# Kernel optimization log

Hardware: AMD Instinct MI355X
Metric: run time of the kernel (lower is better)

The kernel has to match this reference:

```python
import math
import jax, jax.numpy as jnp
import numpy as np

N, E = 100000, 1600000
F_IN, HID, CLS, H = 128, 64, 40, 2  # per-head channels C = HID = 64, concat width = H*HID = 128


def _lin_params(key, fan_in, fan_out):
    kw, kb = jax.random.split(key)
    s = 1.0 / math.sqrt(fan_in)
    W = jax.random.uniform(kw, (fan_in, fan_out), minval=-s, maxval=s, dtype=jnp.float32)
    b = jax.random.uniform(kb, (fan_out,), minval=-s, maxval=s, dtype=jnp.float32)
    return W, b


def setup_inputs() -> dict:
    key = jax.random.key(0)
    ks = jax.random.split(key, 12)
    x = jax.random.normal(ks[0], (N, F_IN), dtype=jnp.float32)
    edge_index = jax.random.randint(ks[1], (2, E), 0, N, dtype=jnp.int64)
    inp = {"x": x, "edge_index": edge_index}
    # layer 1: in=F_IN(128) -> H*HID(128); layer 2: in=H*HID(128) -> H*HID(128)
    names = ["q1", "k1", "v1", "s1", "q2", "k2", "v2", "s2"]
    fans = [(F_IN, H * HID)] * 4 + [(H * HID, H * HID)] * 4
    for i, (nm, (fi, fo)) in enumerate(zip(names, fans)):
        W, b = _lin_params(ks[2 + i], fi, fo)
        inp["W" + nm] = W
        inp["b" + nm] = b
    Wlin, blin = _lin_params(ks[10], H * HID, CLS)
    inp["Wlin"], inp["blin"] = Wlin, blin
    return inp


def _tconv(x, src, dst, Wq, bq, Wk, bk, Wv, bv, Ws, bs):
    # PyG TransformerConv (concat=True, beta=False, edge_dim=None, root_weight=True)
    n = x.shape[0]
    q = (x @ Wq + bq).reshape(n, H, HID)
    k = (x @ Wk + bk).reshape(n, H, HID)
    v = (x @ Wv + bv).reshape(n, H, HID)
    # per-edge attention score: q_i (dst) dot k_j (src), per head
    alpha = jnp.einsum("ehc,ehc->eh", q[dst], k[src]) / math.sqrt(HID)  # [E, H]
    # segment softmax over incoming edges of each dst node
    m = jax.ops.segment_max(alpha, dst, num_segments=n)
    a = jnp.exp(alpha - m[dst])
    denom = jax.ops.segment_sum(a, dst, num_segments=n)
    a = a / (denom[dst] + 1e-16)
    # weighted scatter-aggregate of values
    msg = v[src] * a[:, :, None]  # [E, H, HID]
    out = jax.ops.segment_sum(msg, dst, num_segments=n).reshape(n, H * HID)
    return out + x @ Ws + bs  # root/skip connection


def reference(x, edge_index, Wq1, bq1, Wk1, bk1, Wv1, bv1, Ws1, bs1,
              Wq2, bq2, Wk2, bk2, Wv2, bv2, Ws2, bs2, Wlin, blin):
    src, dst = edge_index[0], edge_index[1]
    h = _tconv(x, src, dst, Wq1, bq1, Wk1, bk1, Wv1, bv1, Ws1, bs1)
    h = jax.nn.elu(h)  # dropout is identity in eval mode
    h = _tconv(h, src, dst, Wq2, bq2, Wk2, bk2, Wv2, bv2, Ws2, bs2)
    return h @ Wlin + blin  # [N, CLS]
```

## Files before the change

### kernel.cpp

```cpp
#include <hip/hip_runtime.h>
#include <math.h>

#define NNODES 100000
#define NEDGES 1600000
#define FD 128
#define NCLS 40
#define NB_SCAN ((NNODES + 1023) / 1024)

typedef __attribute__((ext_vector_type(8))) short short8v;
typedef __attribute__((ext_vector_type(4))) float f32x4;

__device__ __forceinline__ unsigned short f32_to_bf16_rne(float f) {
    unsigned int u = __float_as_uint(f);
    unsigned int r = u + 0x7fff + ((u >> 16) & 1);
    return (unsigned short)(r >> 16);
}
__device__ __forceinline__ float bf16_to_f32(unsigned short h) {
    return __uint_as_float(((unsigned int)h) << 16);
}


__global__ void detect_kernel(const long long* __restrict__ ei, int* __restrict__ flag_is32) {
    int t = blockIdx.x * blockDim.x + threadIdx.x;
    size_t idx = (size_t)t * (NEDGES / 4096);
    long long v = ei[idx];
    if (v < 0 || v >= NNODES) atomicOr(flag_is32, 1);
}

__device__ __forceinline__ void load_edge(const void* eiv, int is32, int e, int& s, int& d) {
    if (is32) {
        const int* p = (const int*)eiv;
        s = p[e]; d = p[NEDGES + e];
    } else {
        const long long* p = (const long long*)eiv;
        s = (int)p[e]; d = (int)p[NEDGES + e];
    }
}


__global__ void hist_kernel(const void* __restrict__ eiv, const int* __restrict__ flag_is32,
                            int* __restrict__ row_ptr) {
    int is32 = *flag_is32;
    int e = blockIdx.x * blockDim.x + threadIdx.x;
    if (e < NEDGES) {
        int s, d;
        load_edge(eiv, is32, e, s, d);
        atomicAdd(&row_ptr[d + 1], 1);
    }
}

__global__ __launch_bounds__(1024) void scan_blk(int* __restrict__ row_ptr,
                                                 int* __restrict__ cursor,
                                                 int* __restrict__ blk_tot) {
    __shared__ int wtot[16];
    __shared__ int woff[16];
    int t = threadIdx.x, lane = t & 63, wid = t >> 6;
    int i = blockIdx.x * 1024 + t;
    int c = (i < NNODES) ? row_ptr[1 + i] : 0;
    int x = c;
    #pragma unroll
    for (int off = 1; off < 64; off <<= 1) {
        int y = __shfl_up(x, off, 64);
        if (lane >= off) x += y;
    }
    if (lane == 63) wtot[wid] = x;
    __syncthreads();
    if (t < 16) {
        int v = wtot[t];
        #pragma unroll
        for (int off = 1; off < 16; off <<= 1) {
            int y = __shfl_up(v, off, 64);
            if (t >= off) v += y;
        }
        woff[t] = v;
    }
    __syncthreads();
    int excl = (wid == 0) ? 0 : woff[wid - 1];
    int incl = x + excl;
    if (i < NNODES) {
        row_ptr[1 + i] = incl;
        cursor[i]      = incl - c;
    }
    if (t == 0) blk_tot[blockIdx.x] = woff[15];
}

__global__ void scan_tops(const int* __restrict__ blk_tot, int* __restrict__ blk_off) {
    __shared__ int s[128];
    int t = threadIdx.x;
    int c0 = (t < NB_SCAN) ? blk_tot[t] : 0;
    s[t] = c0;
    __syncthreads();
    for (int d = 1; d < 128; d <<= 1) {
        int v = (t >= d) ? s[t - d] : 0;
        __syncthreads();
        s[t] += v;
        __syncthreads();
    }
    if (t < NB_SCAN) blk_off[t] = s[t] - c0;
}

__global__ __launch_bounds__(1024) void scan_add(int* __restrict__ row_ptr,
                                                 int* __restrict__ cursor,
                                                 const int* __restrict__ blk_off) {
    int i = blockIdx.x * 1024 + threadIdx.x;
    if (i < NNODES) {
        int o = blk_off[blockIdx.x];
        row_ptr[1 + i] += o;
        cursor[i]      += o;
    }
}

__global__ void fill_kernel(const void* __restrict__ eiv, const int* __restrict__ flag_is32,
                            int* __restrict__ cursor, int* __restrict__ src_sorted) {
    int is32 = *flag_is32;
    int e = blockIdx.x * blockDim.x + threadIdx.x;
    if (e < NEDGES) {
        int s, d;
        load_edge(eiv, is32, e, s, d);
        int pos = atomicAdd(&cursor[d], 1);
        src_sorted[pos] = s;
    }
}


__global__ void pack_w(const float* __restrict__ W, short* __restrict__ Whi,
                       short* __restrict__ Wlo, int slot) {
    int lane = threadIdx.x;
    int ctkk = blockIdx.x;
    int ct = ctkk >> 2, kk = ctkk & 3;
    int col = ct * 16 + (lane & 15);
    int k0 = kk * 32 + (lane >> 4) * 8;
    short8v h, l;
    #pragma unroll
    for (int j = 0; j < 8; j++) {
        float v = W[(size_t)(k0 + j) * FD + col];
        unsigned short hh = f32_to_bf16_rne(v);
        float rem = v - bf16_to_f32(hh);
        h[j] = (short)hh;
        l[j] = (short)f32_to_bf16_rne(rem);
    }
    size_t o = ((size_t)slot * 32 + ctkk) * 512 + (size_t)lane * 8;
    *(short8v*)(Whi + o) = h;
    *(short8v*)(Wlo + o) = l;
}


__global__ __launch_bounds__(256) void proj_gemm_mfma(
    const float* __restrict__ X,
    const short* __restrict__ Whi, const short* __restrict__ Wlo,
    const float* __restrict__ b0, const float* __restrict__ b1,
    const float* __restrict__ b2, const float* __restrict__ b3,
    float* __restrict__ Q, unsigned short* __restrict__ KV, float* __restrict__ SKIP)
{
    int wid = threadIdx.x >> 6, lane = threadIdx.x & 63;
    int rowbase = blockIdx.x * 64 + wid * 16;
    int r = lane & 15, q = lane >> 4;
    int row = rowbase + r;

    short8v xh[4], xl[4];
    if (row < NNODES) {
        const float* xp = X + (size_t)row * FD + q * 8;
        #pragma unroll
        for (int kk = 0; kk < 4; kk++) {
            float4 v0 = *(const float4*)(xp + kk * 32);
            float4 v1 = *(const float4*)(xp + kk * 32 + 4);
            float vv[8] = {v0.x, v0.y, v0.z, v0.w, v1.x, v1.y, v1.z, v1.w};
            #pragma unroll
            for (int j = 0; j < 8; j++) {
                unsigned short h = f32_to_bf16_rne(vv[j]);
                float rem = vv[j] - bf16_to_f32(h);
                xh[kk][j] = (short)h;
                xl[kk][j] = (short)f32_to_bf16_rne(rem);
            }
        }
    } else {
        short8v z = {0, 0, 0, 0, 0, 0, 0, 0};
        #pragma unroll
        for (int kk = 0; kk < 4; kk++) { xh[kk] = z; xl[kk] = z; }
    }

    #pragma unroll
    for (int pt = 0; pt < 4; pt++) {
        const float* bias = (pt == 0) ? b0 : (pt == 1) ? b1 : (pt == 2) ? b2 : b3;
        #pragma unroll
        for (int ct = 0; ct < 8; ct++) {
            const short* wp = Whi + ((size_t)(pt * 8 + ct) * 4) * 512 + (size_t)lane * 8;
            const short* lp = Wlo + ((size_t)(pt * 8 + ct) * 4) * 512 + (size_t)lane * 8;
            f32x4 acc = {0.f, 0.f, 0.f, 0.f};
            #pragma unroll
            for (int kk = 0; kk < 4; kk++) {
                short8v bh = *(const short8v*)(wp + kk * 512);
                short8v bl = *(const short8v*)(lp + kk * 512);
                acc = __builtin_amdgcn_mfma_f32_16x16x32_bf16(xh[kk], bh, acc, 0, 0, 0);
                acc = __builtin_amdgcn_mfma_f32_16x16x32_bf16(xl[kk], bh, acc, 0, 0, 0);
                acc = __builtin_amdgcn_mfma_f32_16x16x32_bf16(xh[kk], bl, acc, 0, 0, 0);
            }
            float bb = bias[ct * 16 + r];
            int e = ct * 16 + r;
            #pragma unroll
            for (int j = 0; j < 4; j++) {
                int ro = rowbase + q * 4 + j;
                if (ro < NNODES) {
                    float val = acc[j] + bb;
                    if (pt == 0)      Q[(size_t)ro * FD + e] = val;
                    else if (pt == 1) KV[(size_t)ro * 256 + 2 * e]     = f32_to_bf16_rne(val);
                    else if (pt == 2) KV[(size_t)ro * 256 + 2 * e + 1] = f32_to_bf16_rne(val);
                    else              SKIP[(size_t)ro * FD + e] = val;
                }
            }
        }
    }
}


__global__ __launch_bounds__(256) void agg_kernel(
    const float* __restrict__ Q, const unsigned short* __restrict__ KV,
    const float* __restrict__ SKIP, float* __restrict__ OUT,
    const int* __restrict__ row_ptr, const int* __restrict__ src_sorted, int apply_elu)
{
    int wid  = threadIdx.x >> 6;
    int lane = threadIdx.x & 63;
    int node = blockIdx.x * 4 + wid;
    if (node >= NNODES) return;
    size_t rb = (size_t)node * FD;
    float2 q = *(const float2*)(Q + rb + 2 * lane);
    q.x *= 0.125f; q.y *= 0.125f;
    float m = -INFINITY, s = 0.f;
    float accx = 0.f, accy = 0.f;
    int e0 = row_ptr[node], e1 = row_ptr[node + 1];

#define EDGE_UPD(W)                                          \
    {                                                        \
        float kx = bf16_to_f32((W).x & 0xffffu);             \
        float vx = bf16_to_f32((W).x >> 16);                 \
        float ky = bf16_to_f32((W).y & 0xffffu);             \
        float vy = bf16_to_f32((W).y >> 16);                 \
        float p = q.x * kx + q.y * ky;                       \
        p += __shfl_xor(p, 1, 64);                           \
        p += __shfl_xor(p, 2, 64);                           \
        p += __shfl_xor(p, 4, 64);                           \
        p += __shfl_xor(p, 8, 64);                           \
        p += __shfl_xor(p, 16, 64);                          \
        float mn   = fmaxf(m, p);                            \
        float corr = __expf(m - mn);                         \
        float w    = __expf(p - mn);                         \
        s    = s * corr + w;                                 \
        accx = accx * corr + w * vx;                         \
        accy = accy * corr + w * vy;                         \
        m = mn;                                              \
    }

    for (int base = e0; base < e1; base += 4) {
        int nrem = e1 - base;
        int j0 = src_sorted[base];
        int j1 = src_sorted[nrem > 1 ? base + 1 : base];
        int j2 = src_sorted[nrem > 2 ? base + 2 : base];
        int j3 = src_sorted[nrem > 3 ? base + 3 : base];
        uint2 w0 = *(const uint2*)((const unsigned int*)(KV + (size_t)j0 * 256) + 2 * lane);
        uint2 w1 = *(const uint2*)((const unsigned int*)(KV + (size_t)j1 * 256) + 2 * lane);
        uint2 w2 = *(const uint2*)((const unsigned int*)(KV + (size_t)j2 * 256) + 2 * lane);
        uint2 w3 = *(const uint2*)((const unsigned int*)(KV + (size_t)j3 * 256) + 2 * lane);
        EDGE_UPD(w0)
        if (nrem > 1) EDGE_UPD(w1)
        if (nrem > 2) EDGE_UPD(w2)
        if (nrem > 3) EDGE_UPD(w3)
    }
#undef EDGE_UPD

    float r = 1.f / (s + 1e-16f);
    float2 sk = *(const float2*)(SKIP + rb + 2 * lane);
    float ox = accx * r + sk.x;
    float oy = accy * r + sk.y;
    if (apply_elu) {
        ox = (ox > 0.f) ? ox : (__expf(ox) - 1.f);
        oy = (oy > 0.f) ? oy : (__expf(oy) - 1.f);
    }
    *(float2*)(OUT + rb + 2 * lane) = make_float2(ox, oy);
}


__global__ void final_lin(const float* __restrict__ H, const float* __restrict__ Wl,
                          const float* __restrict__ bl, float* __restrict__ out)
{
    __shared__ float ws[FD * NCLS];
    __shared__ float xs[8][FD + 1];
    int tx = threadIdx.x;
    int ty = threadIdx.y;
    int t = ty * NCLS + tx;
    for (int i = t; i < FD * NCLS; i += 320) ws[i] = Wl[i];
    int row = blockIdx.x * 8;
    for (int i = t; i < 8 * FD; i += 320) {
        int r = i >> 7, c = i & 127;
        xs[r][c] = (row + r < NNODES) ? H[(size_t)(row + r) * FD + c] : 0.f;
    }
    __syncthreads();
    float acc = bl[tx];
    #pragma unroll
    for (int k = 0; k < FD; k++) acc += xs[ty][k] * ws[k * NCLS + tx];
    if (row + ty < NNODES) out[(size_t)(row + ty) * NCLS + tx] = acc;
}


extern "C" void kernel_launch(void* const* d_in, const int* in_sizes, int n_in,
                              void* d_out, int out_size, void* d_ws, size_t ws_size,
                              hipStream_t stream) {
    const float* x  = (const float*)d_in[0];
    const void*  ei = d_in[1];
    const float* Wq1 = (const float*)d_in[2],  *bq1 = (const float*)d_in[3];
    const float* Wk1 = (const float*)d_in[4],  *bk1 = (const float*)d_in[5];
    const float* Wv1 = (const float*)d_in[6],  *bv1 = (const float*)d_in[7];
    const float* Ws1 = (const float*)d_in[8],  *bs1 = (const float*)d_in[9];
    const float* Wq2 = (const float*)d_in[10], *bq2 = (const float*)d_in[11];
    const float* Wk2 = (const float*)d_in[12], *bk2 = (const float*)d_in[13];
    const float* Wv2 = (const float*)d_in[14], *bv2 = (const float*)d_in[15];
    const float* Ws2 = (const float*)d_in[16], *bs2 = (const float*)d_in[17];
    const float* Wlin = (const float*)d_in[18], *blin = (const float*)d_in[19];
    float* out = (float*)d_out;

    const size_t BUFE = (size_t)NNODES * FD;
    float* Qb = (float*)d_ws;
    float* Cb = Qb + BUFE;
    float* Sb = Cb + BUFE;
    unsigned short* KVb = (unsigned short*)(Sb + BUFE);
    int* row_ptr    = (int*)(KVb + (size_t)NNODES * 256);
    int* cursor     = row_ptr + (NNODES + 1);
    int* src_sorted = cursor + NNODES;
    int* flag_is32  = src_sorted + NEDGES;
    int* blk_tot    = flag_is32 + 1;
    int* blk_off    = blk_tot + NB_SCAN;
    uintptr_t pal = ((uintptr_t)(blk_off + NB_SCAN) + 15) & ~(uintptr_t)15;
    short* Whi = (short*)pal;
    short* Wlo = Whi + 8 * 16384;

    const float* Ws[8] = {Wq1, Wk1, Wv1, Ws1, Wq2, Wk2, Wv2, Ws2};
    for (int s = 0; s < 8; s++)
        pack_w<<<32, 64, 0, stream>>>(Ws[s], Whi, Wlo, s);

    hipMemsetAsync(row_ptr, 0, (NNODES + 1) * sizeof(int), stream);
    hipMemsetAsync(flag_is32, 0, sizeof(int), stream);
    detect_kernel<<<16, 256, 0, stream>>>((const long long*)ei, flag_is32);
    hist_kernel<<<(NEDGES + 255) / 256, 256, 0, stream>>>(ei, flag_is32, row_ptr);
    scan_blk<<<NB_SCAN, 1024, 0, stream>>>(row_ptr, cursor, blk_tot);
    scan_tops<<<1, 128, 0, stream>>>(blk_tot, blk_off);
    scan_add<<<NB_SCAN, 1024, 0, stream>>>(row_ptr, cursor, blk_off);
    fill_kernel<<<(NEDGES + 255) / 256, 256, 0, stream>>>(ei, flag_is32, cursor, src_sorted);

    int pgrid = (NNODES + 63) / 64;

    proj_gemm_mfma<<<pgrid, 256, 0, stream>>>(x, Whi, Wlo,
        bq1, bk1, bv1, bs1, Qb, KVb, Sb);
    agg_kernel<<<(NNODES + 3) / 4, 256, 0, stream>>>(Qb, KVb, Sb, Qb,
        row_ptr, src_sorted, 1);

    proj_gemm_mfma<<<pgrid, 256, 0, stream>>>(Qb, Whi + 4 * 16384, Wlo + 4 * 16384,
        bq2, bk2, bv2, bs2, Cb, KVb, Sb);
    agg_kernel<<<(NNODES + 3) / 4, 256, 0, stream>>>(Cb, KVb, Sb, Cb,
        row_ptr, src_sorted, 0);

    final_lin<<<(NNODES + 7) / 8, dim3(NCLS, 8), 0, stream>>>(Cb, Wlin, blin, out);
}
```

Measured before the change: 947.0 us.

## Process two edges per wavefront in agg kernel and drop online softmax max

The aggregation kernel splits each 64-lane wavefront into two 32-lane halves. Each half handles a different edge and loads 16-byte uint4 K/V chunks, where each lane previously loaded 8 bytes. The online-softmax running max and its rescaling are removed, so each edge needs one exp and four shuffles instead of two exps and five. A final cross-half shuffle combines the partial sums. This removes the serial max dependency and halves the shuffle reductions per edge, but without max subtraction exp can overflow when attention scores are large.

Result: faster. 906.7 us (-4.2%).

```diff
diff --git a/kernel.cpp b/kernel.cpp
--- a/kernel.cpp
+++ b/kernel.cpp
@@ -220,62 +220,72 @@
 {
     int wid  = threadIdx.x >> 6;
     int lane = threadIdx.x & 63;
+    int half = lane >> 5;
+    int sub  = lane & 31;
     int node = blockIdx.x * 4 + wid;
     if (node >= NNODES) return;
     size_t rb = (size_t)node * FD;
-    float2 q = *(const float2*)(Q + rb + 2 * lane);
-    q.x *= 0.125f; q.y *= 0.125f;
-    float m = -INFINITY, s = 0.f;
-    float accx = 0.f, accy = 0.f;
+
+    float4 q4 = *(const float4*)(Q + rb + sub * 4);
+    q4.x *= 0.125f; q4.y *= 0.125f; q4.z *= 0.125f; q4.w *= 0.125f;
+
+    float s = 0.f;
+    float4 acc = make_float4(0.f, 0.f, 0.f, 0.f);
     int e0 = row_ptr[node], e1 = row_ptr[node + 1];
-
-#define EDGE_UPD(W)                                          \
-    {                                                        \
-        float kx = bf16_to_f32((W).x & 0xffffu);             \
-        float vx = bf16_to_f32((W).x >> 16);                 \
-        float ky = bf16_to_f32((W).y & 0xffffu);             \
-        float vy = bf16_to_f32((W).y >> 16);                 \
-        float p = q.x * kx + q.y * ky;                       \
-        p += __shfl_xor(p, 1, 64);                           \
-        p += __shfl_xor(p, 2, 64);                           \
-        p += __shfl_xor(p, 4, 64);                           \
-        p += __shfl_xor(p, 8, 64);                           \
-        p += __shfl_xor(p, 16, 64);                          \
-        float mn   = fmaxf(m, p);                            \
-        float corr = __expf(m - mn);                         \
-        float w    = __expf(p - mn);                         \
-        s    = s * corr + w;                                 \
-        accx = accx * corr + w * vx;                         \
-        accy = accy * corr + w * vy;                         \
-        m = mn;                                              \
+    const uint4* KV4 = (const uint4*)KV;
+
+#define PAIR_UPD(EID)                                                          \
+    {                                                                          \
+        int eid = (EID);                                                       \
+        int valid = eid < e1;                                                  \
+        int j = src_sorted[valid ? eid : e1 - 1];                              \
+        uint4 wv = KV4[(size_t)j * 32 + sub];                                  \
+        float kx = __uint_as_float(wv.x << 16);                                \
+        float vx = __uint_as_float(wv.x & 0xffff0000u);                        \
+        float ky = __uint_as_float(wv.y << 16);                                \
+        float vy = __uint_as_float(wv.y & 0xffff0000u);                        \
+        float kz = __uint_as_float(wv.z << 16);                                \
+        float vz = __uint_as_float(wv.z & 0xffff0000u);                        \
+        float kw = __uint_as_float(wv.w << 16);                                \
+        float vw = __uint_as_float(wv.w & 0xffff0000u);                        \
+        float p = q4.x * kx + q4.y * ky + q4.z * kz + q4.w * kw;               \
+        p += __shfl_xor(p, 1, 64);                                             \
+        p += __shfl_xor(p, 2, 64);                                             \
+        p += __shfl_xor(p, 4, 64);                                             \
+        p += __shfl_xor(p, 8, 64);           \
+        float w = valid ? __expf(p) : 0.f;                                     \
+        s += w;                                                                \
+        acc.x += w * vx; acc.y += w * vy;                                      \
+        acc.z += w * vz; acc.w += w * vw;                                      \
     }
 
     for (int base = e0; base < e1; base += 4) {
-        int nrem = e1 - base;
-        int j0 = src_sorted[base];
-        int j1 = src_sorted[nrem > 1 ? base + 1 : base];
-        int j2 = src_sorted[nrem > 2 ? base + 2 : base];
-        int j3 = src_sorted[nrem > 3 ? base + 3 : base];
-        uint2 w0 = *(const uint2*)((const unsigned int*)(KV + (size_t)j0 * 256) + 2 * lane);
-        uint2 w1 = *(const uint2*)((const unsigned int*)(KV + (size_t)j1 * 256) + 2 * lane);
-        uint2 w2 = *(const uint2*)((const unsigned int*)(KV + (size_t)j2 * 256) + 2 * lane);
-        uint2 w3 = *(const uint2*)((const unsigned int*)(KV + (size_t)j3 * 256) + 2 * lane);
-        EDGE_UPD(w0)
-        if (nrem > 1) EDGE_UPD(w1)
-        if (nrem > 2) EDGE_UPD(w2)
-        if (nrem > 3) EDGE_UPD(w3)
-    }
-#undef EDGE_UPD
-
-    float r = 1.f / (s + 1e-16f);
-    float2 sk = *(const float2*)(SKIP + rb + 2 * lane);
-    float ox = accx * r + sk.x;
-    float oy = accy * r + sk.y;
-    if (apply_elu) {
-        ox = (ox > 0.f) ? ox : (__expf(ox) - 1.f);
-        oy = (oy > 0.f) ? oy : (__expf(oy) - 1.f);
-    }
-    *(float2*)(OUT + rb + 2 * lane) = make_float2(ox, oy);
+        PAIR_UPD(base + half)
+        PAIR_UPD(base + 2 + half)
+    }
+#undef PAIR_UPD
+
+    s += __shfl_xor(s, 32, 64);
+    acc.x += __shfl_xor(acc.x, 32, 64);
+    acc.y += __shfl_xor(acc.y, 32, 64);
+    acc.z += __shfl_xor(acc.z, 32, 64);
+    acc.w += __shfl_xor(acc.w, 32, 64);
+
+    if (half == 0) {
+        float r = 1.f / (s + 1e-16f);
+        float4 sk = *(const float4*)(SKIP + rb + sub * 4);
+        float ox = acc.x * r + sk.x;
+        float oy = acc.y * r + sk.y;
+        float oz = acc.z * r + sk.z;
+        float ow = acc.w * r + sk.w;
+        if (apply_elu) {
+            ox = (ox > 0.f) ? ox : (__expf(ox) - 1.f);
+            oy = (oy > 0.f) ? oy : (__expf(oy) - 1.f);
+            oz = (oz > 0.f) ? oz : (__expf(oz) - 1.f);
+            ow = (ow > 0.f) ? ow : (__expf(ow) - 1.f);
+        }
+        *(float4*)(OUT + rb + sub * 4) = make_float4(ox, oy, oz, ow);
+    }
 }
 
 
```
